# Kernel optimization log

Hardware: AMD Instinct MI355X
Metric: run time of the kernel (lower is better)

## Reference

```python
import jax, jax.numpy as jnp
import numpy as np

D = 128
N_SRC = 50000
N_DST = 50000
E = 640000
NEG_SLOPE = 0.01  # torch LeakyReLU default


def _lrelu(x):
    return jax.nn.leaky_relu(x, NEG_SLOPE)


def setup_inputs() -> dict:
    key = jax.random.key(0)
    ks = jax.random.split(key, 12)
    s = 1.0 / np.sqrt(D)
    return {
        "feat_src": jax.random.normal(ks[0], (N_SRC, D), jnp.float32),
        "feat_dst": jax.random.normal(ks[1], (N_DST, D), jnp.float32),
        "src_idx": jax.random.randint(ks[2], (E,), 0, N_SRC, jnp.int32),
        "dst_idx": jax.random.randint(ks[3], (E,), 0, N_DST, jnp.int32),
        "W_src": jax.random.uniform(ks[4], (D, D), jnp.float32, -s, s),
        "b_src": jnp.zeros((D,), jnp.float32),
        "W_dst": jax.random.uniform(ks[5], (D, D), jnp.float32, -s, s),
        "b_dst": jnp.zeros((D,), jnp.float32),
        "W_a1": jax.random.uniform(ks[6], (D, D), jnp.float32, -s, s),
        "b_a1": jnp.zeros((D,), jnp.float32),
        "W_a2": jax.random.uniform(ks[7], (D, 1), jnp.float32, -s, s),
        "b_a2": jnp.zeros((1,), jnp.float32),
        "W_out": jax.random.uniform(ks[8], (D, D), jnp.float32, -s, s),
        "b_out": jnp.zeros((D,), jnp.float32),
    }


def reference(feat_src, feat_dst, src_idx, dst_idx,
              W_src, b_src, W_dst, b_dst,
              W_a1, b_a1, W_a2, b_a2, W_out, b_out):
    n_dst = feat_dst.shape[0]
    # node projections (dropout is identity in eval mode)
    hs = feat_src @ W_src + b_src            # [n_src, d]
    hd = feat_dst @ W_dst + b_dst            # [n_dst, d]
    # u_add_v: per-edge feature
    e = hs[src_idx] + hd[dst_idx]            # [E, d]
    # attention MLP: LeakyReLU -> Linear -> LeakyReLU -> Linear(d->1)
    s = _lrelu(_lrelu(e) @ W_a1 + b_a1) @ W_a2 + b_a2  # [E, 1]
    s = s[:, 0]
    # edge softmax grouped by destination node (numerically stable)
    m = jax.ops.segment_max(s, dst_idx, num_segments=n_dst)
    ex = jnp.exp(s - m[dst_idx])
    denom = jax.ops.segment_sum(ex, dst_idx, num_segments=n_dst)
    alpha = ex / denom[dst_idx]              # [E]
    # scale messages and scatter-sum to dst nodes
    n_f = jax.ops.segment_sum(alpha[:, None] * e, dst_idx, num_segments=n_dst)
    return _lrelu(n_f @ W_out + b_out)       # [n_dst, d]
```

## Files before the change

### kernel.cpp

```cpp
#include <hip/hip_runtime.h>
#include <math.h>

#define DD 128
#define NEG 0.01f
#define SCHUNK 4096

typedef __attribute__((ext_vector_type(8))) _Float16 half8;
typedef __attribute__((ext_vector_type(4))) float f32x4;

__device__ __forceinline__ float lrelu(float x){ return x > 0.f ? x : NEG * x; }

__device__ __forceinline__ unsigned short h2u(_Float16 h){
    union { _Float16 h; unsigned short u; } v; v.h = h; return v.u;
}
__device__ __forceinline__ _Float16 u2h(unsigned short u){
    union { unsigned short u; _Float16 h; } v; v.u = u; return v.h;
}

__device__ __forceinline__ half8 h8max(half8 x, half8 y){
#if __has_builtin(__builtin_elementwise_max)
    return __builtin_elementwise_max(x, y);
#else
    half8 r;
    #pragma unroll
    for (int i = 0; i < 8; i++) r[i] = x[i] > y[i] ? x[i] : y[i];
    return r;
#endif
}

__global__ void hist_pack(const int* dst, int* deg, int* rank, int E, int nhist,
                          const float* Wa1, const float* Wsrc,
                          const float* Wdst, const float* Wout,
                          unsigned short* wpack){
    const int bid = blockIdx.x;
    if (bid < nhist){
        int i = bid * 256 + threadIdx.x;
        if (i < E) rank[i] = atomicAdd(&deg[dst[i]], 1);
    } else {
        int i = (bid - nhist) * 256 + threadIdx.x;
        if (i >= 4 * 16384) return;
        int seg = i >> 14, t = i & 16383;
        int j = t & 7, lane = (t >> 3) & 63, nt = (t >> 9) & 7, kc = t >> 12;
        int k = kc * 32 + (lane >> 4) * 8 + j;
        int n = nt * 16 + (lane & 15);
        const float* W = (seg == 0) ? Wa1 : (seg == 1) ? Wsrc : (seg == 2) ? Wdst : Wout;
        wpack[i] = h2u((_Float16)W[k * DD + n]);
    }
}

__global__ __launch_bounds__(1024) void scan1(const int* deg, int* part, int n){
    __shared__ int wsum[16];
    const int tid = threadIdx.x;
    const int lane = tid & 63, wid = tid >> 6;
    int i4 = blockIdx.x * SCHUNK + tid * 4;
    int4 v = make_int4(0, 0, 0, 0);
    if (i4 + 3 < n) v = *(const int4*)(deg + i4);
    else {
        if (i4 + 0 < n) v.x = deg[i4 + 0];
        if (i4 + 1 < n) v.y = deg[i4 + 1];
        if (i4 + 2 < n) v.z = deg[i4 + 2];
        if (i4 + 3 < n) v.w = deg[i4 + 3];
    }
    int t = v.x + v.y + v.z + v.w;
    #pragma unroll
    for (int off = 1; off < 64; off <<= 1) t += __shfl_xor(t, off, 64);
    if (lane == 0) wsum[wid] = t;
    __syncthreads();
    if (tid == 0){
        int s = 0;
        #pragma unroll
        for (int j = 0; j < 16; j++) s += wsum[j];
        part[blockIdx.x] = s;
    }
}

__global__ __launch_bounds__(1024) void scan2(const int* deg, const int* part,
        int* row_off, int n, int nchunks){
    __shared__ int wsum[16];
    const int tid = threadIdx.x;
    const int lane = tid & 63, wid = tid >> 6;
    const int b = blockIdx.x;
    int carry = 0;
    for (int j = 0; j < b; j++) carry += part[j];
    int i4 = b * SCHUNK + tid * 4;
    int4 v = make_int4(0, 0, 0, 0);
    if (i4 + 3 < n) v = *(const int4*)(deg + i4);
    else {
        if (i4 + 0 < n) v.x = deg[i4 + 0];
        if (i4 + 1 < n) v.y = deg[i4 + 1];
        if (i4 + 2 < n) v.z = deg[i4 + 2];
        if (i4 + 3 < n) v.w = deg[i4 + 3];
    }
    int tsum = v.x + v.y + v.z + v.w;
    int x = tsum;
    #pragma unroll
    for (int off = 1; off < 64; off <<= 1){
        int t = __shfl_up(x, off, 64);
        if (lane >= off) x += t;
    }
    if (lane == 63) wsum[wid] = x;
    __syncthreads();
    int wprefix = 0;
    #pragma unroll
    for (int j = 0; j < 16; j++) if (j < wid) wprefix += wsum[j];
    int excl = carry + wprefix + (x - tsum);
    if (i4 + 3 < n){
        int4 o;
        o.x = excl; o.y = excl + v.x; o.z = o.y + v.y; o.w = o.z + v.z;
        *(int4*)(row_off + i4) = o;
    } else {
        int a = excl;
        if (i4 + 0 < n){ row_off[i4 + 0] = a; a += v.x; }
        if (i4 + 1 < n){ row_off[i4 + 1] = a; a += v.y; }
        if (i4 + 2 < n){ row_off[i4 + 2] = a; a += v.z; }
        if (i4 + 3 < n){ row_off[i4 + 3] = a; }
    }
    if (b == 0 && tid == 0){
        int tot = 0;
        for (int j = 0; j < nchunks; j++) tot += part[j];
        row_off[n] = tot;
    }
}

__global__ __launch_bounds__(256) void scatter_lin2(
        const int* src, const int* dst, const int* row_off, const int* rank,
        unsigned int* pairs, int E, int nsc,
        const float* X1, const unsigned short* W1, const float* b1,
        unsigned short* Yb1, int n1, int g1,
        const float* X2, const unsigned short* W2, const float* b2,
        unsigned short* Yb2, int n2){
    __shared__ unsigned short sB[16384];
    const int tid = threadIdx.x;
    if (blockIdx.x < nsc){
        int i = blockIdx.x * 256 + tid;
        if (i < E){
            unsigned int d = (unsigned int)dst[i];
            unsigned int s = (unsigned int)src[i];
            pairs[row_off[d] + rank[i]] = (d << 16) | s;
        }
        return;
    }
    const int lb = blockIdx.x - nsc;
    const int second = (lb >= g1);
    const float* X = second ? X2 : X1;
    const unsigned short* W = second ? W2 : W1;
    const float* b = second ? b2 : b1;
    unsigned short* Yb = second ? Yb2 : Yb1;
    const int nrows = second ? n2 : n1;
    const int bidx = second ? (lb - g1) : lb;
    {
        const uint4* g = (const uint4*)W;
        uint4* l = (uint4*)sB;
        #pragma unroll
        for (int t = 0; t < 8; t++) l[tid + 256 * t] = g[tid + 256 * t];
    }
    const int wave = tid >> 6, lane = tid & 63;
    const int qd = lane >> 4, ln16 = lane & 15;
    const int row0 = bidx * 128 + wave * 32;
    int r0 = row0 + ln16;       if (r0 >= nrows) r0 = nrows - 1;
    int r1 = row0 + 16 + ln16;  if (r1 >= nrows) r1 = nrows - 1;
    f32x4 acc[2][8];
    #pragma unroll
    for (int rt = 0; rt < 2; rt++)
        #pragma unroll
        for (int nt = 0; nt < 8; nt++)
            acc[rt][nt] = (f32x4){0.f, 0.f, 0.f, 0.f};
    __syncthreads();
    #pragma unroll
    for (int kc = 0; kc < 4; kc++){
        const int koff = kc * 32 + qd * 8;
        half8 a[2];
        const float* px[2] = {X + (size_t)r0 * DD + koff, X + (size_t)r1 * DD + koff};
        #pragma unroll
        for (int rt = 0; rt < 2; rt++){
            float4 v0 = *(const float4*)(px[rt]);
            float4 v1 = *(const float4*)(px[rt] + 4);
            a[rt][0] = (_Float16)v0.x; a[rt][1] = (_Float16)v0.y;
            a[rt][2] = (_Float16)v0.z; a[rt][3] = (_Float16)v0.w;
            a[rt][4] = (_Float16)v1.x; a[rt][5] = (_Float16)v1.y;
            a[rt][6] = (_Float16)v1.z; a[rt][7] = (_Float16)v1.w;
        }
        #pragma unroll
        for (int nt = 0; nt < 8; nt++){
            const int fi = (((kc << 3) + nt) << 6 | lane) << 3;
            half8 bw = *(const half8*)&sB[fi];
            acc[0][nt] = __builtin_amdgcn_mfma_f32_16x16x32_f16(a[0], bw, acc[0][nt], 0, 0, 0);
            acc[1][nt] = __builtin_amdgcn_mfma_f32_16x16x32_f16(a[1], bw, acc[1][nt], 0, 0, 0);
        }
    }
    #pragma unroll
    for (int nt = 0; nt < 8; nt++){
        const int col = nt * 16 + ln16;
        const float bv = b[col];
        #pragma unroll
        for (int rt = 0; rt < 2; rt++){
            #pragma unroll
            for (int r = 0; r < 4; r++){
                int row = row0 + rt * 16 + qd * 4 + r;
                if (row < nrows){
                    float y = acc[rt][nt][r] + bv;
                    Yb[(size_t)row * DD + col] = h2u((_Float16)y);
                }
            }
        }
    }
}

__device__ __forceinline__ half8 afrag_from(half8 a, half8 b){
    half8 s = a + b;
    return h8max(s, s * (_Float16)NEG);
}

__global__ __launch_bounds__(512) void edge_score_mfma(
        const unsigned short* hs_h, const unsigned short* hd_h,
        const unsigned int* pairs,
        const unsigned short* wa1p, const float* ba1,
        const float* Wa2, const float* ba2,
        float* s_w, int E){
    __shared__ unsigned short sB[16384];
    const int tid = threadIdx.x;
    {
        const uint4* g = (const uint4*)wa1p;
        uint4* l = (uint4*)sB;
        #pragma unroll
        for (int t = 0; t < 4; t++) l[tid + 512 * t] = g[tid + 512 * t];
    }
    int nblk = gridDim.x;
    int q = nblk >> 3, r = nblk & 7;
    int x = blockIdx.x & 7, y = blockIdx.x >> 3;
    int bswz = (x < r ? x * (q + 1) : r * (q + 1) + (x - r) * q) + y;
    const int wave = tid >> 6, lane = tid & 63;
    const int qd = lane >> 4, ln16 = lane & 15;
    const int e0 = bswz * 256 + wave * 32;
    float b1v[8], w2v[8];
    #pragma unroll
    for (int nt = 0; nt < 8; nt++){
        b1v[nt] = ba1[nt * 16 + ln16];
        w2v[nt] = Wa2[nt * 16 + ln16];
    }
    __syncthreads();
    for (int rt = 0; rt < 2; rt++){
        int eid = e0 + rt * 16 + ln16;
        if (eid >= E) eid = E - 1;
        const unsigned int pp = pairs[eid];
        const unsigned int si = pp & 0xffffu, di = pp >> 16;
        f32x4 acc[8];
        #pragma unroll
        for (int nt = 0; nt < 8; nt++)
            acc[nt] = (f32x4){b1v[nt], b1v[nt], b1v[nt], b1v[nt]};
        #pragma unroll
        for (int kc = 0; kc < 4; kc++){
            const int koff = kc * 32 + qd * 8;
            half8 af = afrag_from(*(const half8*)(hs_h + (size_t)si * DD + koff),
                                  *(const half8*)(hd_h + (size_t)di * DD + koff));
            #pragma unroll
            for (int nt = 0; nt < 8; nt++){
                half8 bf = *(const half8*)&sB[(((kc << 3) + nt) << 6 | lane) << 3];
                acc[nt] = __builtin_amdgcn_mfma_f32_16x16x32_f16(af, bf, acc[nt], 0, 0, 0);
            }
        }
        float p[4] = {0.f, 0.f, 0.f, 0.f};
        #pragma unroll
        for (int nt = 0; nt < 8; nt++)
            #pragma unroll
            for (int r2 = 0; r2 < 4; r2++){
                float z = acc[nt][r2];
                z = fmaxf(z, NEG * z);
                p[r2] += z * w2v[nt];
            }
        #pragma unroll
        for (int r2 = 0; r2 < 4; r2++){
            float v = p[r2];
            #pragma unroll
            for (int off = 1; off < 16; off <<= 1) v += __shfl_xor(v, off, 64);
            p[r2] = __expf(v);
        }
        if (ln16 == 0){
            int row = e0 + rt * 16 + qd * 4;
            #pragma unroll
            for (int r2 = 0; r2 < 4; r2++)
                if (row + r2 < E) s_w[row + r2] = p[r2];
        }
    }
}

__global__ __launch_bounds__(512) void agg_lin(
        const unsigned short* hs_h, const unsigned short* hd_h,
        const int* row_off, const unsigned int* pairs, const float* s_w,
        const unsigned short* wout, const float* bout,
        float* Y, int n_dst){
    __shared__ unsigned short sB[16384];
    __shared__ unsigned short rbuf[2048];
    const int tid = threadIdx.x;
    {
        const uint4* g = (const uint4*)wout;
        uint4* l = (uint4*)sB;
        #pragma unroll
        for (int t = 0; t < 4; t++) l[tid + 512 * t] = g[tid + 512 * t];
    }
    const int wave = tid >> 6, lane = tid & 63;
    const int w = blockIdx.x * 8 + wave;
    const int hf = lane >> 5, l32 = lane & 31;
    int beg = 0, end = 0;
    if (w < n_dst){ beg = row_off[w]; end = row_off[w + 1]; }
    float4 acc = make_float4(0.f, 0.f, 0.f, 0.f);
    float sa = 0.f;
    int e = beg;
    for (; e + 7 < end; e += 8){
        int rows[4]; float wv[4]; ushort4 uv[4];
        #pragma unroll
        for (int j = 0; j < 4; j++){
            int ee = e + 2 * j + hf;
            rows[j] = (int)(pairs[ee] & 0xffffu);
            wv[j] = s_w[ee];
        }
        #pragma unroll
        for (int j = 0; j < 4; j++)
            uv[j] = *(const ushort4*)(hs_h + (size_t)rows[j] * DD + l32 * 4);
        #pragma unroll
        for (int j = 0; j < 4; j++){
            acc.x += wv[j] * (float)u2h(uv[j].x);
            acc.y += wv[j] * (float)u2h(uv[j].y);
            acc.z += wv[j] * (float)u2h(uv[j].z);
            acc.w += wv[j] * (float)u2h(uv[j].w);
            sa += wv[j];
        }
    }
    for (; e < end; e += 4){
        int ee0 = e + hf;          int ee1 = e + 2 + hf;
        int ec0 = ee0 < end ? ee0 : end - 1;
        int ec1 = ee1 < end ? ee1 : end - 1;
        int r0 = (int)(pairs[ec0] & 0xffffu), r1 = (int)(pairs[ec1] & 0xffffu);
        float wv0 = (ee0 < end) ? s_w[ec0] : 0.f;
        float wv1 = (ee1 < end) ? s_w[ec1] : 0.f;
        ushort4 u0 = *(const ushort4*)(hs_h + (size_t)r0 * DD + l32 * 4);
        ushort4 u1 = *(const ushort4*)(hs_h + (size_t)r1 * DD + l32 * 4);
        acc.x += wv0 * (float)u2h(u0.x) + wv1 * (float)u2h(u1.x);
        acc.y += wv0 * (float)u2h(u0.y) + wv1 * (float)u2h(u1.y);
        acc.z += wv0 * (float)u2h(u0.z) + wv1 * (float)u2h(u1.z);
        acc.w += wv0 * (float)u2h(u0.w) + wv1 * (float)u2h(u1.w);
        sa += wv0 + wv1;
    }
    acc.x += __shfl_xor(acc.x, 32, 64);
    acc.y += __shfl_xor(acc.y, 32, 64);
    acc.z += __shfl_xor(acc.z, 32, 64);
    acc.w += __shfl_xor(acc.w, 32, 64);
    sa    += __shfl_xor(sa, 32, 64);
    const float inv = (end > beg) ? 1.f / sa : 0.f;
    if (hf == 0 && w < n_dst){
        float hx = 0.f, hy = 0.f, hz = 0.f, hw = 0.f;
        if (end > beg){
            ushort4 hu = *(const ushort4*)(hd_h + (size_t)w * DD + l32 * 4);
            hx = (float)u2h(hu.x); hy = (float)u2h(hu.y);
            hz = (float)u2h(hu.z); hw = (float)u2h(hu.w);
        }
        ushort4 hv;
        hv.x = h2u((_Float16)(acc.x * inv + hx));
        hv.y = h2u((_Float16)(acc.y * inv + hy));
        hv.z = h2u((_Float16)(acc.z * inv + hz));
        hv.w = h2u((_Float16)(acc.w * inv + hw));
        int wb = wave * 256 + ((l32 * 8) ^ ((wave & 7) << 4));
        *(ushort4*)((char*)rbuf + wb) = hv;
    }
    __syncthreads();
    {
        const int nt = wave;
        const int qd = lane >> 4, ln16 = lane & 15;
        f32x4 c = (f32x4){0.f, 0.f, 0.f, 0.f};
        #pragma unroll
        for (int kc = 0; kc < 4; kc++){
            int rb = ln16 * 256 + ((kc * 64 + qd * 16) ^ ((ln16 & 7) << 4));
            half8 af = *(const half8*)((const char*)rbuf + rb);
            half8 bf = *(const half8*)&sB[(((kc << 3) + nt) << 6 | lane) << 3];
            c = __builtin_amdgcn_mfma_f32_16x16x32_f16(af, bf, c, 0, 0, 0);
        }
        const int col = nt * 16 + ln16;
        const float bv = bout[col];
        #pragma unroll
        for (int r = 0; r < 4; r++){
            int row = qd * 4 + r;
            int node = blockIdx.x * 8 + row;
            if (row < 8 && node < n_dst){
                float y = c[r] + bv;
                Y[(size_t)node * DD + col] = lrelu(y);
            }
        }
    }
}

extern "C" void kernel_launch(void* const* d_in, const int* in_sizes, int n_in,
                              void* d_out, int out_size, void* d_ws, size_t ws_size,
                              hipStream_t stream){
    const float* feat_src = (const float*)d_in[0];
    const float* feat_dst = (const float*)d_in[1];
    const int*   src_idx  = (const int*)d_in[2];
    const int*   dst_idx  = (const int*)d_in[3];
    const float* W_src = (const float*)d_in[4];
    const float* b_src = (const float*)d_in[5];
    const float* W_dst = (const float*)d_in[6];
    const float* b_dst = (const float*)d_in[7];
    const float* W_a1  = (const float*)d_in[8];
    const float* b_a1  = (const float*)d_in[9];
    const float* W_a2  = (const float*)d_in[10];
    const float* b_a2  = (const float*)d_in[11];
    const float* W_out = (const float*)d_in[12];
    const float* b_out = (const float*)d_in[13];
    const int n_src = in_sizes[0] / DD;
    const int n_dst = in_sizes[1] / DD;
    const int E = in_sizes[2];
    const int nchunks = (n_dst + SCHUNK - 1) / SCHUNK;

    char* p = (char*)d_ws;
    unsigned short* hs_h = (unsigned short*)p;  p += (size_t)n_src * DD * 2;
    unsigned short* hd_h = (unsigned short*)p;  p += (size_t)n_dst * DD * 2;
    unsigned short* wpack = (unsigned short*)p; p += 4 * 16384 * 2;
    float* s_w = (float*)p;                     p += (size_t)E * 4;
    unsigned int* pairs = (unsigned int*)p;     p += (size_t)E * 4;
    int* rank = (int*)p;                        p += (size_t)E * 4;
    int* deg = (int*)p;                         p += (size_t)n_dst * 4;
    int* part = (int*)p;                        p += 64 * 4;
    int* row_off = (int*)p;                     p += ((size_t)n_dst + 1) * 4;
    float* nf = (float*)d_out;

    const unsigned short* wa1p = wpack;
    const unsigned short* wsrc = wpack + 1 * 16384;
    const unsigned short* wdst = wpack + 2 * 16384;
    const unsigned short* wout = wpack + 3 * 16384;

    hipMemsetAsync(deg, 0, (size_t)n_dst * 4, stream);
    const int nhist = (E + 255) / 256;
    const int npack = (4 * 16384 + 255) / 256;
    hist_pack<<<nhist + npack, 256, 0, stream>>>(dst_idx, deg, rank, E, nhist,
                                                 W_a1, W_src, W_dst, W_out, wpack);
    scan1<<<nchunks, 1024, 0, stream>>>(deg, part, n_dst);
    scan2<<<nchunks, 1024, 0, stream>>>(deg, part, row_off, n_dst, nchunks);
    const int nsc = (E + 255) / 256;
    const int g1 = (n_src + 127) / 128;
    const int g2 = (n_dst + 127) / 128;
    scatter_lin2<<<nsc + g1 + g2, 256, 0, stream>>>(src_idx, dst_idx, row_off, rank,
                                                    pairs, E, nsc,
                                                    feat_src, wsrc, b_src, hs_h, n_src, g1,
                                                    feat_dst, wdst, b_dst, hd_h, n_dst);
    edge_score_mfma<<<(E + 255) / 256, 512, 0, stream>>>(hs_h, hd_h, pairs, wa1p, b_a1,
                                                         W_a2, b_a2, s_w, E);
    agg_lin<<<(n_dst + 7) / 8, 512, 0, stream>>>(hs_h, hd_h, row_off, pairs, s_w,
                                                 wout, b_out, nf, n_dst);
}
```

Measured before the change: 267.7 us.

## Move node projections into histogram kernel and prefetch edge indices in aggregation

The src and dst node projection GEMMs move out of the scatter kernel and into the first histogram kernel. Each projection block now packs its fp32 weight straight into shared memory as fp16, so the global pre-pack of those two weights is dropped. The scatter becomes a small standalone kernel, which lets the projections overlap the degree histogram instead of waiting behind the scan. The aggregation loop also software-prefetches the next batch of pair indices and weights while the current gathers are in flight, at the cost of more registers and a per-block repack of W into LDS.

```diff
diff --git a/kernel.cpp b/kernel.cpp
--- a/kernel.cpp
+++ b/kernel.cpp
@@ -28,23 +28,106 @@
 #endif
 }
 
-__global__ void hist_pack(const int* dst, int* deg, int* rank, int E, int nhist,
-                          const float* Wa1, const float* Wsrc,
-                          const float* Wdst, const float* Wout,
-                          unsigned short* wpack){
+__global__ __launch_bounds__(256) void hist_pack_lin2(
+        const int* dst, int* deg, int* rank, int E, int nhist, int npack,
+        const float* Wa1, const float* Wout, unsigned short* wpack,
+        const float* X1, const float* W1, const float* b1,
+        unsigned short* Yb1, int n1, int g1,
+        const float* X2, const float* W2, const float* b2,
+        unsigned short* Yb2, int n2){
+    __shared__ unsigned short sB[16384];
+    const int tid = threadIdx.x;
     const int bid = blockIdx.x;
     if (bid < nhist){
-        int i = bid * 256 + threadIdx.x;
+        int i = bid * 256 + tid;
         if (i < E) rank[i] = atomicAdd(&deg[dst[i]], 1);
-    } else {
-        int i = (bid - nhist) * 256 + threadIdx.x;
-        if (i >= 4 * 16384) return;
-        int seg = i >> 14, t = i & 16383;
-        int j = t & 7, lane = (t >> 3) & 63, nt = (t >> 9) & 7, kc = t >> 12;
-        int k = kc * 32 + (lane >> 4) * 8 + j;
-        int n = nt * 16 + (lane & 15);
-        const float* W = (seg == 0) ? Wa1 : (seg == 1) ? Wsrc : (seg == 2) ? Wdst : Wout;
-        wpack[i] = h2u((_Float16)W[k * DD + n]);
+        return;
+    }
+    if (bid < nhist + npack){
+        int i = (bid - nhist) * 256 + tid;
+        if (i < 2 * 16384){
+            int seg = i >> 14, t = i & 16383;
+            int j = t & 7, lane = (t >> 3) & 63, nt = (t >> 9) & 7, kc = t >> 12;
+            int k = kc * 32 + (lane >> 4) * 8 + j;
+            int n = nt * 16 + (lane & 15);
+            const float* W = (seg == 0) ? Wa1 : Wout;
+            wpack[i] = h2u((_Float16)W[k * DD + n]);
+        }
+        return;
+    }
+    const int lb = bid - nhist - npack;
+    const int second = (lb >= g1);
+    const float* X = second ? X2 : X1;
+    const float* W = second ? W2 : W1;
+    const float* b = second ? b2 : b1;
+    unsigned short* Yb = second ? Yb2 : Yb1;
+    const int nrows = second ? n2 : n1;
+    const int bidx = second ? (lb - g1) : lb;
+    #pragma unroll
+    for (int c = 0; c < 8; c++){
+        int e = (c * 256 + tid) * 8;
+        int k = e >> 7, n0 = e & 127;
+        float4 v0 = *(const float4*)(W + e);
+        float4 v1 = *(const float4*)(W + e + 4);
+        float vv[8] = {v0.x, v0.y, v0.z, v0.w, v1.x, v1.y, v1.z, v1.w};
+        int kc = k >> 5, jj = k & 7, lhi = (k >> 3) & 3;
+        #pragma unroll
+        for (int j = 0; j < 8; j++){
+            int nn = n0 + j;
+            int lane2 = (lhi << 4) | (nn & 15);
+            int idx = (((((kc << 3) | (nn >> 4)) << 6) | lane2) << 3) | jj;
+            sB[idx] = h2u((_Float16)vv[j]);
+        }
+    }
+    const int wave = tid >> 6, lane = tid & 63;
+    const int qd = lane >> 4, ln16 = lane & 15;
+    const int row0 = bidx * 128 + wave * 32;
+    int r0 = row0 + ln16;       if (r0 >= nrows) r0 = nrows - 1;
+    int r1 = row0 + 16 + ln16;  if (r1 >= nrows) r1 = nrows - 1;
+    f32x4 acc[2][8];
+    #pragma unroll
+    for (int rt = 0; rt < 2; rt++)
+        #pragma unroll
+        for (int nt = 0; nt < 8; nt++)
+            acc[rt][nt] = (f32x4){0.f, 0.f, 0.f, 0.f};
+    __syncthreads();
+    #pragma unroll
+    for (int kc = 0; kc < 4; kc++){
+        const int koff = kc * 32 + qd * 8;
+        half8 a[2];
+        const float* px[2] = {X + (size_t)r0 * DD + koff, X + (size_t)r1 * DD + koff};
+        #pragma unroll
+        for (int rt = 0; rt < 2; rt++){
+            float4 v0 = *(const float4*)(px[rt]);
+            float4 v1 = *(const float4*)(px[rt] + 4);
+            a[rt][0] = (_Float16)v0.x; a[rt][1] = (_Float16)v0.y;
+            a[rt][2] = (_Float16)v0.z; a[rt][3] = (_Float16)v0.w;
+            a[rt][4] = (_Float16)v1.x; a[rt][5] = (_Float16)v1.y;
+            a[rt][6] = (_Float16)v1.z; a[rt][7] = (_Float16)v1.w;
+        }
+        #pragma unroll
+        for (int nt = 0; nt < 8; nt++){
+            const int fi = (((kc << 3) + nt) << 6 | lane) << 3;
+            half8 bw = *(const half8*)&sB[fi];
+            acc[0][nt] = __builtin_amdgcn_mfma_f32_16x16x32_f16(a[0], bw, acc[0][nt], 0, 0, 0);
+            acc[1][nt] = __builtin_amdgcn_mfma_f32_16x16x32_f16(a[1], bw, acc[1][nt], 0, 0, 0);
+        }
+    }
+    #pragma unroll
+    for (int nt = 0; nt < 8; nt++){
+        const int col = nt * 16 + ln16;
+        const float bv = b[col];
+        #pragma unroll
+        for (int rt = 0; rt < 2; rt++){
+            #pragma unroll
+            for (int r = 0; r < 4; r++){
+                int row = row0 + rt * 16 + qd * 4 + r;
+                if (row < nrows){
+                    float y = acc[rt][nt][r] + bv;
+                    Yb[(size_t)row * DD + col] = h2u((_Float16)y);
+                }
+            }
+        }
     }
 }
 
@@ -122,87 +205,12 @@
     }
 }
 
-__global__ __launch_bounds__(256) void scatter_lin2(
-        const int* src, const int* dst, const int* row_off, const int* rank,
-        unsigned int* pairs, int E, int nsc,
-        const float* X1, const unsigned short* W1, const float* b1,
-        unsigned short* Yb1, int n1, int g1,
-        const float* X2, const unsigned short* W2, const float* b2,
-        unsigned short* Yb2, int n2){
-    __shared__ unsigned short sB[16384];
-    const int tid = threadIdx.x;
-    if (blockIdx.x < nsc){
-        int i = blockIdx.x * 256 + tid;
-        if (i < E){
-            unsigned int d = (unsigned int)dst[i];
-            unsigned int s = (unsigned int)src[i];
-            pairs[row_off[d] + rank[i]] = (d << 16) | s;
-        }
-        return;
-    }
-    const int lb = blockIdx.x - nsc;
-    const int second = (lb >= g1);
-    const float* X = second ? X2 : X1;
-    const unsigned short* W = second ? W2 : W1;
-    const float* b = second ? b2 : b1;
-    unsigned short* Yb = second ? Yb2 : Yb1;
-    const int nrows = second ? n2 : n1;
-    const int bidx = second ? (lb - g1) : lb;
-    {
-        const uint4* g = (const uint4*)W;
-        uint4* l = (uint4*)sB;
-        #pragma unroll
-        for (int t = 0; t < 8; t++) l[tid + 256 * t] = g[tid + 256 * t];
-    }
-    const int wave = tid >> 6, lane = tid & 63;
-    const int qd = lane >> 4, ln16 = lane & 15;
-    const int row0 = bidx * 128 + wave * 32;
-    int r0 = row0 + ln16;       if (r0 >= nrows) r0 = nrows - 1;
-    int r1 = row0 + 16 + ln16;  if (r1 >= nrows) r1 = nrows - 1;
-    f32x4 acc[2][8];
-    #pragma unroll
-    for (int rt = 0; rt < 2; rt++)
-        #pragma unroll
-        for (int nt = 0; nt < 8; nt++)
-            acc[rt][nt] = (f32x4){0.f, 0.f, 0.f, 0.f};
-    __syncthreads();
-    #pragma unroll
-    for (int kc = 0; kc < 4; kc++){
-        const int koff = kc * 32 + qd * 8;
-        half8 a[2];
-        const float* px[2] = {X + (size_t)r0 * DD + koff, X + (size_t)r1 * DD + koff};
-        #pragma unroll
-        for (int rt = 0; rt < 2; rt++){
-            float4 v0 = *(const float4*)(px[rt]);
-            float4 v1 = *(const float4*)(px[rt] + 4);
-            a[rt][0] = (_Float16)v0.x; a[rt][1] = (_Float16)v0.y;
-            a[rt][2] = (_Float16)v0.z; a[rt][3] = (_Float16)v0.w;
-            a[rt][4] = (_Float16)v1.x; a[rt][5] = (_Float16)v1.y;
-            a[rt][6] = (_Float16)v1.z; a[rt][7] = (_Float16)v1.w;
-        }
-        #pragma unroll
-        for (int nt = 0; nt < 8; nt++){
-            const int fi = (((kc << 3) + nt) << 6 | lane) << 3;
-            half8 bw = *(const half8*)&sB[fi];
-            acc[0][nt] = __builtin_amdgcn_mfma_f32_16x16x32_f16(a[0], bw, acc[0][nt], 0, 0, 0);
-            acc[1][nt] = __builtin_amdgcn_mfma_f32_16x16x32_f16(a[1], bw, acc[1][nt], 0, 0, 0);
-        }
-    }
-    #pragma unroll
-    for (int nt = 0; nt < 8; nt++){
-        const int col = nt * 16 + ln16;
-        const float bv = b[col];
-        #pragma unroll
-        for (int rt = 0; rt < 2; rt++){
-            #pragma unroll
-            for (int r = 0; r < 4; r++){
-                int row = row0 + rt * 16 + qd * 4 + r;
-                if (row < nrows){
-                    float y = acc[rt][nt][r] + bv;
-                    Yb[(size_t)row * DD + col] = h2u((_Float16)y);
-                }
-            }
-        }
+__global__ void scatter_pack(const int* src, const int* dst, const int* row_off,
+                             const int* rank, unsigned int* pairs, int E){
+    int i = blockIdx.x * blockDim.x + threadIdx.x;
+    if (i < E){
+        unsigned int d = (unsigned int)dst[i];
+        pairs[row_off[d] + rank[i]] = (d << 16) | (unsigned int)src[i];
     }
 }
 
@@ -306,17 +314,31 @@
     float4 acc = make_float4(0.f, 0.f, 0.f, 0.f);
     float sa = 0.f;
     int e = beg;
-    for (; e + 7 < end; e += 8){
-        int rows[4]; float wv[4]; ushort4 uv[4];
+    int rows[4]; float wv[4];
+    if (e + 7 < end){
         #pragma unroll
         for (int j = 0; j < 4; j++){
             int ee = e + 2 * j + hf;
             rows[j] = (int)(pairs[ee] & 0xffffu);
             wv[j] = s_w[ee];
         }
+    }
+    while (e + 7 < end){
+        ushort4 uv[4];
         #pragma unroll
         for (int j = 0; j < 4; j++)
             uv[j] = *(const ushort4*)(hs_h + (size_t)rows[j] * DD + l32 * 4);
+        const int en = e + 8;
+        int nrows[4]; float nwv[4];
+        const bool more = (en + 7 < end);
+        if (more){
+            #pragma unroll
+            for (int j = 0; j < 4; j++){
+                int ee = en + 2 * j + hf;
+                nrows[j] = (int)(pairs[ee] & 0xffffu);
+                nwv[j] = s_w[ee];
+            }
+        }
         #pragma unroll
         for (int j = 0; j < 4; j++){
             acc.x += wv[j] * (float)u2h(uv[j].x);
@@ -324,6 +346,11 @@
             acc.z += wv[j] * (float)u2h(uv[j].z);
             acc.w += wv[j] * (float)u2h(uv[j].w);
             sa += wv[j];
+        }
+        e = en;
+        if (more){
+            #pragma unroll
+            for (int j = 0; j < 4; j++){ rows[j] = nrows[j]; wv[j] = nwv[j]; }
         }
     }
     for (; e < end; e += 4){
@@ -413,7 +440,7 @@
     char* p = (char*)d_ws;
     unsigned short* hs_h = (unsigned short*)p;  p += (size_t)n_src * DD * 2;
     unsigned short* hd_h = (unsigned short*)p;  p += (size_t)n_dst * DD * 2;
-    unsigned short* wpack = (unsigned short*)p; p += 4 * 16384 * 2;
+    unsigned short* wpack = (unsigned short*)p; p += 2 * 16384 * 2;
     float* s_w = (float*)p;                     p += (size_t)E * 4;
     unsigned int* pairs = (unsigned int*)p;     p += (size_t)E * 4;
     int* rank = (int*)p;                        p += (size_t)E * 4;
@@ -423,24 +450,22 @@
     float* nf = (float*)d_out;
 
     const unsigned short* wa1p = wpack;
-    const unsigned short* wsrc = wpack + 1 * 16384;
-    const unsigned short* wdst = wpack + 2 * 16384;
-    const unsigned short* wout = wpack + 3 * 16384;
+    const unsigned short* wout = wpack + 16384;
 
     hipMemsetAsync(deg, 0, (size_t)n_dst * 4, stream);
     const int nhist = (E + 255) / 256;
-    const int npack = (4 * 16384 + 255) / 256;
-    hist_pack<<<nhist + npack, 256, 0, stream>>>(dst_idx, deg, rank, E, nhist,
-                                                 W_a1, W_src, W_dst, W_out, wpack);
+    const int npack = (2 * 16384 + 255) / 256;
+    const int g1 = (n_src + 127) / 128;
+    const int g2 = (n_dst + 127) / 128;
+    hist_pack_lin2<<<nhist + npack + g1 + g2, 256, 0, stream>>>(
+        dst_idx, deg, rank, E, nhist, npack,
+        W_a1, W_out, wpack,
+        feat_src, W_src, b_src, hs_h, n_src, g1,
+        feat_dst, W_dst, b_dst, hd_h, n_dst);
     scan1<<<nchunks, 1024, 0, stream>>>(deg, part, n_dst);
     scan2<<<nchunks, 1024, 0, stream>>>(deg, part, row_off, n_dst, nchunks);
-    const int nsc = (E + 255) / 256;
-    const int g1 = (n_src + 127) / 128;
-    const int g2 = (n_dst + 127) / 128;
-    scatter_lin2<<<nsc + g1 + g2, 256, 0, stream>>>(src_idx, dst_idx, row_off, rank,
-                                                    pairs, E, nsc,
-                                                    feat_src, wsrc, b_src, hs_h, n_src, g1,
-                                                    feat_dst, wdst, b_dst, hd_h, n_dst);
+    scatter_pack<<<(E + 255) / 256, 256, 0, stream>>>(src_idx, dst_idx, row_off,
+                                                      rank, pairs, E);
     edge_score_mfma<<<(E + 255) / 256, 512, 0, stream>>>(hs_h, hd_h, pairs, wa1p, b_a1,
                                                          W_a2, b_a2, s_w, E);
     agg_lin<<<(n_dst + 7) / 8, 512, 0, stream>>>(hs_h, hd_h, row_off, pairs, s_w,
```

Result: slower. 274.2 us (+2.4%).
